# Performance work log

Hardware: AMD Instinct MI355X
Metric: run time of the kernel (lower is better)

## Reference

```python
import jax, jax.numpy as jnp
import numpy as np

FEATS = [(100, 100), (50, 50), (25, 25), (13, 13)]  # (W, H) per level
BS, NQ, D = 2, 10000, 256
NH, NL, NP, G = 8, 4, 4, 8
HD = D // NH


def grid_sample_bilinear(im, grid):
    """torch.nn.functional.grid_sample(mode='bilinear', padding_mode='zeros', align_corners=False).
    im: [N, C, H, W]; grid: [N, Hg, Wg, 2] in [-1, 1] (x, y). Returns [N, C, Hg, Wg]."""
    N, C, H, W = im.shape
    Hg, Wg = grid.shape[1], grid.shape[2]
    x = (grid[..., 0] + 1.0) * (W * 0.5) - 0.5
    y = (grid[..., 1] + 1.0) * (H * 0.5) - 0.5
    x0 = jnp.floor(x); y0 = jnp.floor(y)
    wx1 = x - x0; wx0 = 1.0 - wx1
    wy1 = y - y0; wy0 = 1.0 - wy1
    imf = im.reshape(N, C, H * W)

    def corner(xi, yi, w):
        inb = (xi >= 0) & (xi < W) & (yi >= 0) & (yi < H)
        xi_c = jnp.clip(xi, 0, W - 1).astype(jnp.int32)
        yi_c = jnp.clip(yi, 0, H - 1).astype(jnp.int32)
        idx = (yi_c * W + xi_c).reshape(N, 1, Hg * Wg)
        vals = jnp.take_along_axis(imf, idx, axis=2).reshape(N, C, Hg, Wg)
        return vals * (w * inb.astype(im.dtype))[:, None]

    out = (corner(x0, y0, wx0 * wy0) + corner(x0 + 1, y0, wx1 * wy0)
           + corner(x0, y0 + 1, wx0 * wy1) + corner(x0 + 1, y0 + 1, wx1 * wy1))
    return out


def setup_inputs() -> dict:
    key = jax.random.key(0)
    ks = jax.random.split(key, 7)
    nv = sum(w * h for (w, h) in FEATS)
    return {
        "query": jax.random.normal(ks[0], (BS, NQ, D), jnp.float32),
        "value": jax.random.normal(ks[1], (BS, nv, NH, HD), jnp.float32),
        "reference_points": jax.random.uniform(ks[2], (BS, NQ, NL, 2), jnp.float32),
        "spatial_shapes": jnp.array(FEATS, jnp.float32),  # rows are (W, H)
        "W_off": jax.random.normal(ks[3], (NH * NL * NP * 2, D), jnp.float32) * 0.02,
        "b_off": jax.random.normal(ks[4], (NH * NL * NP * 2,), jnp.float32) * 0.5,
        "W_attn": jax.random.normal(ks[5], (NH * NL * NP, D), jnp.float32) * 0.02,
        "b_attn": jax.random.normal(ks[6], (NH * NL * NP,), jnp.float32) * 0.02,
    }


def reference(query, value, reference_points, spatial_shapes, W_off, b_off, W_attn, b_attn):
    bs, nq, _ = query.shape
    # sampling offsets: [bs, nq, NH, NL*NP*2] with (level, point, xy) layout
    off = (jnp.einsum('bqd,od->bqo', query, W_off) + b_off).reshape(bs, nq, NH, NL * NP * 2)
    # reference points tiled to the same (level, point, xy) layout
    ref = jnp.broadcast_to(reference_points[:, :, None, :, None, :],
                           (bs, nq, NH, NL, NP, 2)).reshape(bs, nq, NH, NL * NP * 2)
    # offset normalizer: (1/W, 1/H) per level, tiled over points
    inv = 1.0 / spatial_shapes  # [NL, 2]
    norm = jnp.broadcast_to(inv[:, None, :], (NL, NP, 2)).reshape(-1)
    loc = (ref + off * norm) * 2.0 - 1.0  # [bs, nq, NH, NL*NP*2]
    loc = loc.reshape(bs, nq, NH, NL, NP, 2)

    # attention weights: softmax over (NL*NP), then rearranged to [bs*NH, 1, nq/G, NL*G*NP]
    aw = jax.nn.softmax((jnp.einsum('bqd,od->bqo', query, W_attn) + b_attn)
                        .reshape(bs, nq, NH, NL * NP), axis=-1)
    aw = aw.reshape(bs, nq // G, G, NH, NL, NP).transpose(0, 3, 1, 4, 2, 5)
    aw = aw.reshape(bs * NH, 1, nq // G, NL * G * NP)

    # per-level grid_sample
    sizes = [w * h for (w, h) in FEATS]
    starts = np.concatenate([[0], np.cumsum(sizes)]).tolist()
    sampled = []
    for lvl, (Wl, Hl) in enumerate(FEATS):
        val_l = value[:, starts[lvl]:starts[lvl + 1]]  # [bs, Hl*Wl, NH, HD]
        val_l = val_l.transpose(0, 2, 3, 1).reshape(bs * NH, HD, Hl, Wl)
        grid_l = loc[:, :, :, lvl].transpose(0, 2, 1, 3, 4)  # [bs, NH, nq, NP, 2]
        grid_l = grid_l.reshape(bs * NH, nq // G, G * NP, 2)
        sampled.append(grid_sample_bilinear(val_l, grid_l))  # [bs*NH, HD, nq/G, G*NP]
    sv = jnp.concatenate(sampled, axis=-1)  # [bs*NH, HD, nq/G, NL*G*NP]

    out = sv * aw
    # reduce_sum linear (fixed 0/1 weight from init_weights) == sum over levels and points per group slot
    out = out.reshape(bs * NH, HD, nq // G, NL, G, NP).sum(axis=(3, 5))  # [bs*NH, HD, nq/G, G]
    return out.reshape(bs, NH * HD, nq)
```

## Files before the change

kernel.cpp:

```cpp
#include <hip/hip_runtime.h>

#define NQ   10000
#define BSZ  2
#define DIM  256
#define NH   8
#define HD   32
#define NLV  4
#define NPT  4
#define NV   13294
#define MT   (BSZ*NQ)
#define NOUT 384
#define NVAL (BSZ*NV*NH*HD)
#define GEMM_BLOCKS 939
#define PREP_BLOCKS 6647

typedef float    floatx4 __attribute__((ext_vector_type(4)));
typedef int      intx4   __attribute__((ext_vector_type(4)));
typedef __bf16   bf16x8  __attribute__((ext_vector_type(8)));
typedef _Float16 halfx8  __attribute__((ext_vector_type(8)));
typedef _Float16 halfx4  __attribute__((ext_vector_type(4)));

__device__ __forceinline__ unsigned pk_bf16(float lo, float hi) {
  return __builtin_amdgcn_perm(__float_as_uint(hi) + 0x8000u,
                               __float_as_uint(lo) + 0x8000u, 0x07060302);
}

__device__ __forceinline__ unsigned short f32_to_f16_bits(float f) {
  _Float16 h = (_Float16)f;
  return __builtin_bit_cast(unsigned short, h);
}

__global__ __launch_bounds__(256) void gp_kernel(
    const float* __restrict__ query, const float* __restrict__ W_off,
    const float* __restrict__ W_attn,
    const float* __restrict__ b_off, const float* __restrict__ b_attn,
    const float* __restrict__ value,
    _Float16* __restrict__ rawh, _Float16* __restrict__ vf16) {
  const int bid = blockIdx.x;
  const int tid = threadIdx.x;
  if (bid >= GEMM_BLOCKS) {
    int i = (bid - GEMM_BLOCKS) * 256 + tid;
    if (i * 4 < NVAL) {
      floatx4 v = *(const floatx4*)&value[i * 4];
      halfx4 t = { (_Float16)v.x, (_Float16)v.y, (_Float16)v.z, (_Float16)v.w };
      *(uint2*)&vf16[i * 4] = *(const uint2*)&t;
    }
    return;
  }
  __shared__ unsigned short As[64][40];
  __shared__ unsigned short Bs[128][40];
  const int n0 = (bid % 3) * 128;
  const int m0 = (bid / 3) * 64;
  const int wave = tid >> 6;
  const int lane = tid & 63;
  const int quad = lane >> 4;
  const int l16  = lane & 15;
  floatx4 acc[8] = {};
  const int ar = tid >> 2;
  const int ac = (tid & 3) * 8;
  const int br = tid >> 1;
  const int bc = (tid & 1) * 16;
  const float* __restrict__ Wsrc =
      (n0 < 256) ? (W_off + (size_t)n0 * DIM) : (W_attn + (size_t)(n0 - 256) * DIM);

  for (int k0 = 0; k0 < DIM; k0 += 32) {
    {
      int gm = m0 + ar;
      floatx4 a0 = {}, a1 = {};
      if (gm < MT) {
        const float* src = query + (size_t)gm * DIM + k0 + ac;
        a0 = *(const floatx4*)src;
        a1 = *(const floatx4*)(src + 4);
      }
      uint4 ua = { pk_bf16(a0.x, a0.y), pk_bf16(a0.z, a0.w),
                   pk_bf16(a1.x, a1.y), pk_bf16(a1.z, a1.w) };
      *(uint4*)&As[ar][ac] = ua;
    }
    {
      const float* src = Wsrc + (size_t)br * DIM + k0 + bc;
      floatx4 b0 = *(const floatx4*)src;
      floatx4 b1 = *(const floatx4*)(src + 4);
      floatx4 b2 = *(const floatx4*)(src + 8);
      floatx4 b3 = *(const floatx4*)(src + 12);
      uint4 u0 = { pk_bf16(b0.x, b0.y), pk_bf16(b0.z, b0.w),
                   pk_bf16(b1.x, b1.y), pk_bf16(b1.z, b1.w) };
      uint4 u1 = { pk_bf16(b2.x, b2.y), pk_bf16(b2.z, b2.w),
                   pk_bf16(b3.x, b3.y), pk_bf16(b3.z, b3.w) };
      *(uint4*)&Bs[br][bc]     = u0;
      *(uint4*)&Bs[br][bc + 8] = u1;
    }
    __syncthreads();
    bf16x8 a = *(const bf16x8*)&As[wave*16 + l16][quad*8];
    #pragma unroll
    for (int nt = 0; nt < 8; nt++) {
      bf16x8 b = *(const bf16x8*)&Bs[nt*16 + l16][quad*8];
      acc[nt] = __builtin_amdgcn_mfma_f32_16x16x32_bf16(a, b, acc[nt], 0, 0, 0);
    }
    __syncthreads();
  }
  #pragma unroll
  for (int nt = 0; nt < 8; nt++) {
    int gn = n0 + nt*16 + l16;
    float bias = (gn < 256) ? b_off[gn] : b_attn[gn - 256];
    #pragma unroll
    for (int r = 0; r < 4; r++) {
      int gm = m0 + wave*16 + quad*4 + r;
      if (gm < MT) rawh[(size_t)gm*NOUT + gn] = (_Float16)(acc[nt][r] + bias);
    }
  }
}

__global__ __launch_bounds__(256) void sample_kernel(
    const _Float16* __restrict__ rawh, const _Float16* __restrict__ vf16,
    const float* __restrict__ refp, _Float16* __restrict__ tmph) {
  const int b  = blockIdx.y;
  const int q0 = blockIdx.x * 8;
  const int mbase = b * NQ + q0;
  const int tid = threadIdx.x;

  __shared__ int          s_off[64 * 68];
  __shared__ unsigned int s_w  [64 * 34];
  __shared__ float        s_aw [64 * 17];

  const int WLI[4] = {100, 50, 25, 13};
  const int STI[4] = {0, 10000, 12500, 13125};

  float rpx[4], rpy[4];

  #pragma unroll
  for (int it = 0; it < 4; ++it) {
    int slot = it * 256 + tid;
    int ql = slot >> 7, r = slot & 127, h = r >> 4, lp = r & 15, l = lp >> 2, p = lp & 3;
    int m = mbase + ql;
    const _Float16* rp = rawh + (size_t)m * NOUT;
    float offx = (float)rp[h*32 + l*8 + p*2 + 0];
    float offy = (float)rp[h*32 + l*8 + p*2 + 1];
    s_aw[(ql*8 + h)*17 + lp] = (float)rp[256 + h*16 + lp];
    float Wl = (float)WLI[l];
    float rx = refp[(m*NLV + l)*2 + 0];
    float ry = refp[(m*NLV + l)*2 + 1];
    rpx[it] = rx * Wl + offx - 0.5f;
    rpy[it] = ry * Wl + offy - 0.5f;
  }
  __syncthreads();

  if (tid < 64) {
    int base = tid * 17;
    float mx = -1e30f;
    #pragma unroll
    for (int i = 0; i < 16; i++) mx = fmaxf(mx, s_aw[base + i]);
    float s = 0.f;
    float e[16];
    #pragma unroll
    for (int i = 0; i < 16; i++) { e[i] = expf(s_aw[base + i] - mx); s += e[i]; }
    float inv = 1.f / s;
    #pragma unroll
    for (int i = 0; i < 16; i++) s_aw[base + i] = e[i] * inv;
  }
  __syncthreads();

  #pragma unroll
  for (int it = 0; it < 4; ++it) {
    int slot = it * 256 + tid;
    int ql = slot >> 7, r = slot & 127, h = r >> 4, lp = r & 15, l = lp >> 2;
    int rowqh = ql*8 + h;
    float aw = s_aw[rowqh*17 + lp];
    float px = rpx[it], py = rpy[it];
    float x0f = floorf(px), y0f = floorf(py);
    int x0 = (int)x0f, y0 = (int)y0f;
    float wx1 = px - x0f, wx0 = 1.f - wx1;
    float wy1 = py - y0f, wy0 = 1.f - wy1;
    int Wl = WLI[l], STl = STI[l];
    int offs[4]; unsigned short wb[4];
    #pragma unroll
    for (int t = 0; t < 4; ++t) {
      int xi = x0 + (t & 1), yi = y0 + (t >> 1);
      bool inb = (xi >= 0) & (xi < Wl) & (yi >= 0) & (yi < Wl);
      offs[t] = inb ? ((STl + yi*Wl + xi) * 512 + h * 64) : 0;
      float w = inb ? (aw * ((t & 1) ? wx1 : wx0) * ((t >> 1) ? wy1 : wy0)) : 0.f;
      wb[t] = f32_to_f16_bits(w);
    }
    *(intx4*)&s_off[rowqh*68 + lp*4] = *(const intx4*)offs;
    uint2 wp = { (unsigned)wb[0] | ((unsigned)wb[1] << 16),
                 (unsigned)wb[2] | ((unsigned)wb[3] << 16) };
    *(uint2*)&s_w[rowqh*34 + lp*2] = wp;
  }
  __syncthreads();

  const int wv = tid >> 6, lane = tid & 63;
  const int qh = lane >> 5, ql = wv*2 + qh;
  const int h = (lane >> 2) & 7, cq = lane & 3;
  const char* vb = (const char*)vf16 + (size_t)b * (NV*NH*HD*2) + cq * 16;
  floatx4 acc0 = {0.f,0.f,0.f,0.f}, acc1 = {0.f,0.f,0.f,0.f};
  const int orow = (ql*8 + h) * 68, wrow = (ql*8 + h) * 34;
  #pragma unroll 4
  for (int pt = 0; pt < 16; ++pt) {
    intx4 offs = *(const intx4*)&s_off[orow + pt*4];
    uint2 wp   = *(const uint2*)&s_w[wrow + pt*2];
    halfx4 hw  = __builtin_bit_cast(halfx4, wp);
    halfx8 v0 = *(const halfx8*)(vb + offs.x);
    halfx8 v1 = *(const halfx8*)(vb + offs.y);
    halfx8 v2 = *(const halfx8*)(vb + offs.z);
    halfx8 v3 = *(const halfx8*)(vb + offs.w);
    #pragma unroll
    for (int t = 0; t < 4; ++t) {
      halfx8 v = (t==0) ? v0 : (t==1) ? v1 : (t==2) ? v2 : v3;
      float w = (float)hw[t];
      acc0.x += w * (float)v[0];
      acc0.y += w * (float)v[1];
      acc0.z += w * (float)v[2];
      acc0.w += w * (float)v[3];
      acc1.x += w * (float)v[4];
      acc1.y += w * (float)v[5];
      acc1.z += w * (float)v[6];
      acc1.w += w * (float)v[7];
    }
  }
  int m = mbase + ql;
  uint4 st = { __builtin_bit_cast(unsigned, __builtin_amdgcn_cvt_pkrtz(acc0.x, acc0.y)),
               __builtin_bit_cast(unsigned, __builtin_amdgcn_cvt_pkrtz(acc0.z, acc0.w)),
               __builtin_bit_cast(unsigned, __builtin_amdgcn_cvt_pkrtz(acc1.x, acc1.y)),
               __builtin_bit_cast(unsigned, __builtin_amdgcn_cvt_pkrtz(acc1.z, acc1.w)) };
  *(uint4*)&tmph[(size_t)m * DIM + h*HD + cq*8] = st;
}

__global__ __launch_bounds__(256) void transpose_kernel(
    const _Float16* __restrict__ tmph, float* __restrict__ out) {
  __shared__ float tile[32][33];
  const int b  = blockIdx.z;
  const int q0 = blockIdx.x * 32;
  const int c0 = blockIdx.y * 32;
  const int tx = threadIdx.x & 31;
  const int ty = threadIdx.x >> 5;
  #pragma unroll
  for (int i = 0; i < 4; i++) {
    int qq = q0 + ty + i*8;
    tile[ty + i*8][tx] = (qq < NQ) ? (float)tmph[((size_t)b*NQ + qq)*DIM + c0 + tx] : 0.f;
  }
  __syncthreads();
  if (q0 + tx < NQ) {
    #pragma unroll
    for (int i = 0; i < 4; i++) {
      out[((size_t)b*DIM + c0 + ty + i*8)*NQ + q0 + tx] = tile[tx][ty + i*8];
    }
  }
}

extern "C" void kernel_launch(void* const* d_in, const int* in_sizes, int n_in,
                              void* d_out, int out_size, void* d_ws, size_t ws_size,
                              hipStream_t stream) {
  const float* query  = (const float*)d_in[0];
  const float* value  = (const float*)d_in[1];
  const float* refp   = (const float*)d_in[2];
  const float* W_off  = (const float*)d_in[4];
  const float* b_off  = (const float*)d_in[5];
  const float* W_attn = (const float*)d_in[6];
  const float* b_attn = (const float*)d_in[7];
  float* out = (float*)d_out;

  char* ws = (char*)d_ws;
  _Float16* rawh = (_Float16*)ws;
  _Float16* tmph = (_Float16*)(ws + 15360000);
  _Float16* vf16 = (_Float16*)(ws + 25600000);

  hipLaunchKernelGGL(gp_kernel, dim3(GEMM_BLOCKS + PREP_BLOCKS), dim3(256), 0, stream,
                     query, W_off, W_attn, b_off, b_attn, value, rawh, vf16);
  hipLaunchKernelGGL(sample_kernel, dim3(NQ / 8, BSZ), dim3(256), 0, stream,
                     rawh, vf16, refp, tmph);
  hipLaunchKernelGGL(transpose_kernel, dim3(313, 8, 2), dim3(256), 0, stream,
                     tmph, out);
}
```

Before: 167.3 us.

## Pre-cast weights to bf16 and fuse output transpose into sampling kernel

Adds a small kernel that converts W_off and W_attn to bf16 once. The GEMM then reads B fragments straight from global memory instead of staging converted weights through shared memory in every block. The sampling kernel now transposes its results through shared memory and writes fp32 output directly, which removes the fp16 intermediate buffer and the separate transpose kernel. In exchange it adds a launch, issues uncached-pattern global B loads inside the MFMA loop, and makes output stores of 32 bytes per channel row.

```diff
diff --git a/kernel.cpp b/kernel.cpp
--- a/kernel.cpp
+++ b/kernel.cpp
@@ -11,6 +11,7 @@
 #define MT   (BSZ*NQ)
 #define NOUT 384
 #define NVAL (BSZ*NV*NH*HD)
+#define NW   98304
 #define GEMM_BLOCKS 939
 #define PREP_BLOCKS 6647
 
@@ -30,9 +31,20 @@
   return __builtin_bit_cast(unsigned short, h);
 }
 
+__global__ __launch_bounds__(256) void wcast_kernel(
+    const float* __restrict__ W_off, const float* __restrict__ W_attn,
+    unsigned short* __restrict__ Wb) {
+  int j = (blockIdx.x * 256 + threadIdx.x) * 4;
+  if (j < NW) {
+    const float* src = (j < 65536) ? (W_off + j) : (W_attn + (j - 65536));
+    floatx4 v = *(const floatx4*)src;
+    uint2 p = { pk_bf16(v.x, v.y), pk_bf16(v.z, v.w) };
+    *(uint2*)&Wb[j] = p;
+  }
+}
+
 __global__ __launch_bounds__(256) void gp_kernel(
-    const float* __restrict__ query, const float* __restrict__ W_off,
-    const float* __restrict__ W_attn,
+    const float* __restrict__ query, const unsigned short* __restrict__ Wb,
     const float* __restrict__ b_off, const float* __restrict__ b_attn,
     const float* __restrict__ value,
     _Float16* __restrict__ rawh, _Float16* __restrict__ vf16) {
@@ -48,7 +60,6 @@
     return;
   }
   __shared__ unsigned short As[64][40];
-  __shared__ unsigned short Bs[128][40];
   const int n0 = (bid % 3) * 128;
   const int m0 = (bid / 3) * 64;
   const int wave = tid >> 6;
@@ -58,10 +69,7 @@
   floatx4 acc[8] = {};
   const int ar = tid >> 2;
   const int ac = (tid & 3) * 8;
-  const int br = tid >> 1;
-  const int bc = (tid & 1) * 16;
-  const float* __restrict__ Wsrc =
-      (n0 < 256) ? (W_off + (size_t)n0 * DIM) : (W_attn + (size_t)(n0 - 256) * DIM);
+  const unsigned short* __restrict__ wrow = Wb + (size_t)(n0 + l16) * DIM + quad*8;
 
   for (int k0 = 0; k0 < DIM; k0 += 32) {
     {
@@ -76,24 +84,11 @@
                    pk_bf16(a1.x, a1.y), pk_bf16(a1.z, a1.w) };
       *(uint4*)&As[ar][ac] = ua;
     }
-    {
-      const float* src = Wsrc + (size_t)br * DIM + k0 + bc;
-      floatx4 b0 = *(const floatx4*)src;
-      floatx4 b1 = *(const floatx4*)(src + 4);
-      floatx4 b2 = *(const floatx4*)(src + 8);
-      floatx4 b3 = *(const floatx4*)(src + 12);
-      uint4 u0 = { pk_bf16(b0.x, b0.y), pk_bf16(b0.z, b0.w),
-                   pk_bf16(b1.x, b1.y), pk_bf16(b1.z, b1.w) };
-      uint4 u1 = { pk_bf16(b2.x, b2.y), pk_bf16(b2.z, b2.w),
-                   pk_bf16(b3.x, b3.y), pk_bf16(b3.z, b3.w) };
-      *(uint4*)&Bs[br][bc]     = u0;
-      *(uint4*)&Bs[br][bc + 8] = u1;
-    }
     __syncthreads();
     bf16x8 a = *(const bf16x8*)&As[wave*16 + l16][quad*8];
     #pragma unroll
     for (int nt = 0; nt < 8; nt++) {
-      bf16x8 b = *(const bf16x8*)&Bs[nt*16 + l16][quad*8];
+      bf16x8 b = *(const bf16x8*)(wrow + nt*16*DIM + k0);
       acc[nt] = __builtin_amdgcn_mfma_f32_16x16x32_bf16(a, b, acc[nt], 0, 0, 0);
     }
     __syncthreads();
@@ -112,7 +107,7 @@
 
 __global__ __launch_bounds__(256) void sample_kernel(
     const _Float16* __restrict__ rawh, const _Float16* __restrict__ vf16,
-    const float* __restrict__ refp, _Float16* __restrict__ tmph) {
+    const float* __restrict__ refp, float* __restrict__ out) {
   const int b  = blockIdx.y;
   const int q0 = blockIdx.x * 8;
   const int mbase = b * NQ + q0;
@@ -216,33 +211,24 @@
       acc1.w += w * (float)v[7];
     }
   }
-  int m = mbase + ql;
-  uint4 st = { __builtin_bit_cast(unsigned, __builtin_amdgcn_cvt_pkrtz(acc0.x, acc0.y)),
-               __builtin_bit_cast(unsigned, __builtin_amdgcn_cvt_pkrtz(acc0.z, acc0.w)),
-               __builtin_bit_cast(unsigned, __builtin_amdgcn_cvt_pkrtz(acc1.x, acc1.y)),
-               __builtin_bit_cast(unsigned, __builtin_amdgcn_cvt_pkrtz(acc1.z, acc1.w)) };
-  *(uint4*)&tmph[(size_t)m * DIM + h*HD + cq*8] = st;
-}
-
-__global__ __launch_bounds__(256) void transpose_kernel(
-    const _Float16* __restrict__ tmph, float* __restrict__ out) {
-  __shared__ float tile[32][33];
-  const int b  = blockIdx.z;
-  const int q0 = blockIdx.x * 32;
-  const int c0 = blockIdx.y * 32;
-  const int tx = threadIdx.x & 31;
-  const int ty = threadIdx.x >> 5;
-  #pragma unroll
-  for (int i = 0; i < 4; i++) {
-    int qq = q0 + ty + i*8;
-    tile[ty + i*8][tx] = (qq < NQ) ? (float)tmph[((size_t)b*NQ + qq)*DIM + c0 + tx] : 0.f;
-  }
-  __syncthreads();
-  if (q0 + tx < NQ) {
-    #pragma unroll
-    for (int i = 0; i < 4; i++) {
-      out[((size_t)b*DIM + c0 + ty + i*8)*NQ + q0 + tx] = tile[tx][ty + i*8];
-    }
+  __syncthreads();
+  float* s_out = (float*)s_off;
+  {
+    int chb = h*32 + cq*8;
+    #pragma unroll
+    for (int j = 0; j < 4; ++j) s_out[(chb + j)*9 + ql]     = acc0[j];
+    #pragma unroll
+    for (int j = 0; j < 4; ++j) s_out[(chb + 4 + j)*9 + ql] = acc1[j];
+  }
+  __syncthreads();
+  {
+    const int ch = tid;
+    const float* srow = &s_out[ch*9];
+    floatx4 o0 = { srow[0], srow[1], srow[2], srow[3] };
+    floatx4 o1 = { srow[4], srow[5], srow[6], srow[7] };
+    float* dst = out + ((size_t)(b*DIM + ch))*NQ + q0;
+    *(floatx4*)dst       = o0;
+    *(floatx4*)(dst + 4) = o1;
   }
 }
 
@@ -259,14 +245,14 @@
   float* out = (float*)d_out;
 
   char* ws = (char*)d_ws;
-  _Float16* rawh = (_Float16*)ws;
-  _Float16* tmph = (_Float16*)(ws + 15360000);
-  _Float16* vf16 = (_Float16*)(ws + 25600000);
-
+  _Float16*       rawh = (_Float16*)ws;
+  _Float16*       vf16 = (_Float16*)(ws + 15360000);
+  unsigned short* Wb   = (unsigned short*)(ws + 28973056);
+
+  hipLaunchKernelGGL(wcast_kernel, dim3(96), dim3(256), 0, stream,
+                     W_off, W_attn, Wb);
   hipLaunchKernelGGL(gp_kernel, dim3(GEMM_BLOCKS + PREP_BLOCKS), dim3(256), 0, stream,
-                     query, W_off, W_attn, b_off, b_attn, value, rawh, vf16);
+                     query, Wb, b_off, b_attn, value, rawh, vf16);
   hipLaunchKernelGGL(sample_kernel, dim3(NQ / 8, BSZ), dim3(256), 0, stream,
-                     rawh, vf16, refp, tmph);
-  hipLaunchKernelGGL(transpose_kernel, dim3(313, 8, 2), dim3(256), 0, stream,
-                     tmph, out);
-}
+                     rawh, vf16, refp, out);
+}
```

New measurement: 182.5 us. 9.1% more time.
